# Performance work log

Hardware: AMD Instinct MI355X
Metric: run time of the kernel (lower is better)

## Reference

```python
import jax, jax.numpy as jnp
import numpy as np

NEG_SLOPE = 0.2


def gat_conv(h_in, src, dst, W, attn_l, attn_r, num_nodes):
    """DGL-style GATConv: fc -> per-head attention logits -> edge softmax over dst -> scatter-add."""
    H, D = attn_l.shape
    h = (h_in @ W).reshape(num_nodes, H, D)                      # [N,H,D]
    el = jnp.sum(h * attn_l, axis=-1)                            # [N,H]
    er = jnp.sum(h * attn_r, axis=-1)                            # [N,H]
    e = jax.nn.leaky_relu(el[src] + er[dst], NEG_SLOPE)          # [E,H]
    m = jax.ops.segment_max(e, dst, num_segments=num_nodes)      # [N,H]
    m = jnp.where(jnp.isfinite(m), m, 0.0)                       # guard empty segments
    ex = jnp.exp(e - m[dst])                                     # [E,H]
    denom = jax.ops.segment_sum(ex, dst, num_segments=num_nodes) # [N,H]
    a = ex / denom[dst]                                          # [E,H]
    msg = h[src] * a[:, :, None]                                 # [E,H,D]
    out = jax.ops.segment_sum(msg, dst, num_segments=num_nodes)  # [N,H,D]
    return out.reshape(num_nodes, H * D)                         # concat heads


def setup_inputs() -> dict:
    key = jax.random.key(0)
    ks = jax.random.split(key, 12)
    N, E, G = 65536, 1048576, 512
    F_in, H, D = 128, 8, 32
    F_mid = H * D  # 256, concat agg mode
    P = 512
    inp = {
        "node_feats": jax.random.normal(ks[0], (N, F_in), jnp.float32),
        "src": jax.random.randint(ks[1], (E,), 0, N, jnp.int32),
        "dst": jax.random.randint(ks[2], (E,), 0, N, jnp.int32),
        "graph_ids": jnp.sort(jax.random.randint(ks[3], (N,), 0, G, jnp.int32)),
        "num_graphs": G,
        "W0": jax.random.normal(ks[4], (F_in, H * D), jnp.float32) * (1.0 / np.sqrt(F_in)),
        "al0": jax.random.normal(ks[5], (H, D), jnp.float32) * 0.1,
        "ar0": jax.random.normal(ks[6], (H, D), jnp.float32) * 0.1,
        "W1": jax.random.normal(ks[7], (F_mid, H * D), jnp.float32) * (1.0 / np.sqrt(F_mid)),
        "al1": jax.random.normal(ks[8], (H, D), jnp.float32) * 0.1,
        "ar1": jax.random.normal(ks[9], (H, D), jnp.float32) * 0.1,
        "Wd1": jax.random.normal(ks[10], (F_mid, P), jnp.float32) * (1.0 / np.sqrt(F_mid)),
        "bd1": jnp.zeros((P,), jnp.float32),
        "Wd2": jax.random.normal(ks[11], (P, 1), jnp.float32) * (1.0 / np.sqrt(P)),
        "bd2": jnp.zeros((1,), jnp.float32),
    }
    return inp


def reference(node_feats, src, dst, graph_ids, num_graphs,
              W0, al0, ar0, W1, al1, ar1, Wd1, bd1, Wd2, bd2):
    N = node_feats.shape[0]
    # two GATConv message-passing steps with concat head aggregation
    h = gat_conv(node_feats, src, dst, W0, al0, ar0, N)   # [N, 256]
    h = gat_conv(h, src, dst, W1, al1, ar1, N)            # [N, 256]
    # mean readout per graph (AvgPooling)
    sums = jax.ops.segment_sum(h, graph_ids, num_segments=num_graphs)         # [G, 256]
    counts = jax.ops.segment_sum(jnp.ones((N,), h.dtype), graph_ids,
                                 num_segments=num_graphs)                     # [G]
    pooled = sums / jnp.maximum(counts, 1.0)[:, None]
    # predictor MLP: Dense(512, relu) -> Dense(1, linear)
    hidden = jax.nn.relu(pooled @ Wd1 + bd1)
    out = hidden @ Wd2 + bd2                               # [G, 1]
    return out
```

## Files before the change

### kernel.cpp

```cpp
#include <hip/hip_runtime.h>

#define LEAKY 0.2f

typedef unsigned short ushort_t;
typedef __attribute__((ext_vector_type(8))) short short8;
typedef __attribute__((ext_vector_type(4))) float f32x4;

__device__ __forceinline__ unsigned short f2bf(float f) {
  unsigned u = __float_as_uint(f);
  unsigned r = (u + 0x7fff + ((u >> 16) & 1)) >> 16;
  return (unsigned short)r;
}
__device__ __forceinline__ float bf2f(unsigned short u) {
  return __uint_as_float(((unsigned)u) << 16);
}

__global__ void count_k(const int* __restrict__ dst, int* __restrict__ cnt, int E) {
  int base = (blockIdx.x * blockDim.x + threadIdx.x) * 4;
  if (base + 3 < E) {
    int4 d = *(const int4*)(dst + base);
    atomicAdd(&cnt[d.x], 1);
    atomicAdd(&cnt[d.y], 1);
    atomicAdd(&cnt[d.z], 1);
    atomicAdd(&cnt[d.w], 1);
  } else {
    for (int i = base; i < E; ++i) atomicAdd(&cnt[dst[i]], 1);
  }
}

__global__ __launch_bounds__(1024) void scan1_k(int* __restrict__ cnt,
                                                int* __restrict__ ptr,
                                                int* __restrict__ bsum, int N) {
  int t = threadIdx.x;
  int i = blockIdx.x * 1024 + t;
  int v = (i < N) ? cnt[i] : 0;
  if (i < N) cnt[i] = 0;
  int lane = t & 63, w = t >> 6;
  int x = v;
  #pragma unroll
  for (int off = 1; off < 64; off <<= 1) {
    int y = __shfl_up(x, off, 64);
    if (lane >= off) x += y;
  }
  __shared__ int wsum[16];
  if (lane == 63) wsum[w] = x;
  __syncthreads();
  if (t < 16) {
    int s = wsum[t];
    #pragma unroll
    for (int off = 1; off < 16; off <<= 1) {
      int y = __shfl_up(s, off, 16);
      if (t >= off) s += y;
    }
    wsum[t] = s;
  }
  __syncthreads();
  int woff = (w > 0) ? wsum[w - 1] : 0;
  int incl = x + woff;
  if (i < N) ptr[i] = incl - v;
  if (t == 1023) bsum[blockIdx.x] = incl;
}

__global__ __launch_bounds__(1024) void scan23_k(int* __restrict__ ptr,
                                                 const int* __restrict__ bsum,
                                                 int nb, int N, int E) {
  __shared__ int sh[64];
  int t = threadIdx.x;
  if (t < 64) {
    int v = (t < nb) ? bsum[t] : 0;
    int x = v;
    #pragma unroll
    for (int off = 1; off < 64; off <<= 1) {
      int y = __shfl_up(x, off, 64);
      if (t >= off) x += y;
    }
    sh[t] = x - v;
  }
  __syncthreads();
  int i = blockIdx.x * 1024 + t;
  if (i < N) ptr[i] += sh[blockIdx.x];
  if (i == 0) ptr[N] = E;
}

__global__ void fill_k(const int* __restrict__ dst, const int* __restrict__ src,
                       const int* __restrict__ ptr, int* __restrict__ cur,
                       int* __restrict__ adj, int E) {
  int base = (blockIdx.x * blockDim.x + threadIdx.x) * 4;
  if (base + 3 < E) {
    int4 d = *(const int4*)(dst + base);
    int4 s = *(const int4*)(src + base);
    int p0 = atomicAdd(&cur[d.x], 1); adj[ptr[d.x] + p0] = s.x;
    int p1 = atomicAdd(&cur[d.y], 1); adj[ptr[d.y] + p1] = s.y;
    int p2 = atomicAdd(&cur[d.z], 1); adj[ptr[d.z] + p2] = s.z;
    int p3 = atomicAdd(&cur[d.w], 1); adj[ptr[d.w] + p3] = s.w;
  } else {
    for (int i = base; i < E; ++i) {
      int d = dst[i];
      int p = atomicAdd(&cur[d], 1);
      adj[ptr[d] + p] = src[i];
    }
  }
}

__global__ void wsplit2_k(const float* __restrict__ W0, const float* __restrict__ W1,
                          ushort_t* __restrict__ W0h, ushort_t* __restrict__ W1h) {
  int i = blockIdx.x * 256 + threadIdx.x;
  if (i < 256 * 128) {
    int k = i % 128, c = i / 128;
    W0h[i] = f2bf(W0[(long)k * 256 + c]);
  } else {
    int j = i - 256 * 128;
    if (j < 256 * 256) {
      int k = j % 256, c = j / 256;
      W1h[j] = f2bf(W1[(long)k * 256 + c]);
    }
  }
}

#define LDT 40
template <int AF32>
__global__ __launch_bounds__(256) void gemmT_k(const void* __restrict__ Ag_,
                                               const ushort_t* __restrict__ Bh,
                                               const float* __restrict__ alv,
                                               const float* __restrict__ arv,
                                               ushort_t* __restrict__ C,
                                               float* __restrict__ el,
                                               float* __restrict__ er,
                                               int N, int K) {
  __shared__ ushort_t smem[128 * LDT + 256 * LDT];
  ushort_t* As = smem;
  ushort_t* Bs = smem + 128 * LDT;
  int t = threadIdx.x;
  int w = t >> 6, l = t & 63;
  int wv_r = w >> 1, wv_c = w & 1;
  long row0 = (long)blockIdx.x * 128;
  int fr = l & 15;
  int ko = (l >> 4) * 8;
  int crow = (l >> 4) * 4;
  int ar = t >> 1;
  int ak = (t & 1) * 16;
  int bc = t;
  f32x4 acc[4][8] = {};

  for (int k0 = 0; k0 < K; k0 += 32) {
    ushort4 ha[4];
    uint4 a0, a1;
    if (AF32) {
      const float* ap = (const float*)Ag_ + (row0 + ar) * (long)K + k0 + ak;
      float4 v0 = *(const float4*)(ap + 0);
      float4 v1 = *(const float4*)(ap + 4);
      float4 v2 = *(const float4*)(ap + 8);
      float4 v3 = *(const float4*)(ap + 12);
      ha[0] = make_ushort4(f2bf(v0.x), f2bf(v0.y), f2bf(v0.z), f2bf(v0.w));
      ha[1] = make_ushort4(f2bf(v1.x), f2bf(v1.y), f2bf(v1.z), f2bf(v1.w));
      ha[2] = make_ushort4(f2bf(v2.x), f2bf(v2.y), f2bf(v2.z), f2bf(v2.w));
      ha[3] = make_ushort4(f2bf(v3.x), f2bf(v3.y), f2bf(v3.z), f2bf(v3.w));
    } else {
      const ushort_t* ap = (const ushort_t*)Ag_ + (row0 + ar) * (long)K + k0 + ak;
      a0 = *(const uint4*)ap;
      a1 = *(const uint4*)(ap + 8);
    }
    const ushort_t* bp = Bh + (long)bc * K + k0;
    uint4 b0 = *(const uint4*)bp;
    uint4 b1 = *(const uint4*)(bp + 8);
    uint4 b2 = *(const uint4*)(bp + 16);
    uint4 b3 = *(const uint4*)(bp + 24);
    __syncthreads();
    if (AF32) {
      *(ushort4*)&As[ar * LDT + ak + 0] = ha[0];
      *(ushort4*)&As[ar * LDT + ak + 4] = ha[1];
      *(ushort4*)&As[ar * LDT + ak + 8] = ha[2];
      *(ushort4*)&As[ar * LDT + ak + 12] = ha[3];
    } else {
      *(uint4*)&As[ar * LDT + ak] = a0;
      *(uint4*)&As[ar * LDT + ak + 8] = a1;
    }
    *(uint4*)&Bs[bc * LDT + 0] = b0;
    *(uint4*)&Bs[bc * LDT + 8] = b1;
    *(uint4*)&Bs[bc * LDT + 16] = b2;
    *(uint4*)&Bs[bc * LDT + 24] = b3;
    __syncthreads();
    short8 fah[4];
    #pragma unroll
    for (int m = 0; m < 4; ++m)
      fah[m] = *(const short8*)&As[(wv_r * 64 + m * 16 + fr) * LDT + ko];
    #pragma unroll
    for (int n = 0; n < 8; ++n) {
      short8 fb = *(const short8*)&Bs[(wv_c * 128 + n * 16 + fr) * LDT + ko];
      #pragma unroll
      for (int m = 0; m < 4; ++m)
        acc[m][n] = __builtin_amdgcn_mfma_f32_16x16x32_bf16(fah[m], fb, acc[m][n], 0, 0, 0);
    }
  }
  float ala[4], alb[4], ara[4], arb[4];
  #pragma unroll
  for (int hd = 0; hd < 4; ++hd) {
    int hbase = (wv_c * 4 + hd) * 32;
    ala[hd] = alv[hbase + fr];
    alb[hd] = alv[hbase + 16 + fr];
    ara[hd] = arv[hbase + fr];
    arb[hd] = arv[hbase + 16 + fr];
  }
  #pragma unroll
  for (int m = 0; m < 4; ++m) {
    #pragma unroll
    for (int r = 0; r < 4; ++r) {
      long row = row0 + wv_r * 64 + m * 16 + crow + r;
      #pragma unroll
      for (int n = 0; n < 8; ++n)
        C[row * 256 + wv_c * 128 + n * 16 + fr] = f2bf(acc[m][n][r]);
      #pragma unroll
      for (int hd = 0; hd < 4; ++hd) {
        float pel = acc[m][2 * hd][r] * ala[hd] + acc[m][2 * hd + 1][r] * alb[hd];
        float per = acc[m][2 * hd][r] * ara[hd] + acc[m][2 * hd + 1][r] * arb[hd];
        #pragma unroll
        for (int s = 1; s < 16; s <<= 1) {
          pel += __shfl_xor(pel, s);
          per += __shfl_xor(per, s);
        }
        if (fr == 0) {
          el[row * 8 + wv_c * 4 + hd] = pel;
          er[row * 8 + wv_c * 4 + hd] = per;
        }
      }
    }
  }
}

__global__ __launch_bounds__(256) void agg_k(const ushort_t* __restrict__ hb,
                                             const float* __restrict__ el,
                                             const float* __restrict__ er,
                                             const int* __restrict__ ptr,
                                             const int* __restrict__ adj,
                                             ushort_t* __restrict__ oh, int N) {
  int wid = threadIdx.x >> 6;
  int l = threadIdx.x & 63;
  int n = blockIdx.x * 4 + wid;
  if (n >= N) return;
  int beg = ptr[n];
  int deg = ptr[n + 1] - beg;
  long obase = (long)n * 256 + l * 4;
  float4 acc = make_float4(0.f, 0.f, 0.f, 0.f);
  if (deg > 0) {
    int hh = l & 7;
    int eo = l >> 3;
    int hg = l >> 3;
    float erv = er[(long)n * 8 + hh];
    if (deg <= 64) {
      int sid = (l < deg) ? adj[beg + l] : 0;
      int npass = (deg + 7) >> 3;
      float v[8];
      float m = -1e30f;
      #pragma unroll
      for (int p = 0; p < 8; ++p) {
        if (p < npass) {
          int e = p * 8 + eo;
          int s = __shfl(sid, e);
          float vv = -1e30f;
          if (e < deg) {
            vv = el[(long)s * 8 + hh] + erv;
            vv = vv > 0.f ? vv : LEAKY * vv;
          }
          v[p] = vv;
          m = fmaxf(m, vv);
        }
      }
      m = fmaxf(m, __shfl_xor(m, 8));
      m = fmaxf(m, __shfl_xor(m, 16));
      m = fmaxf(m, __shfl_xor(m, 32));
      float ssum = 0.f;
      #pragma unroll
      for (int p = 0; p < 8; ++p) {
        if (p < npass) {
          float ex = (p * 8 + eo < deg) ? __expf(v[p] - m) : 0.f;
          v[p] = ex;
          ssum += ex;
        }
      }
      ssum += __shfl_xor(ssum, 8);
      ssum += __shfl_xor(ssum, 16);
      ssum += __shfl_xor(ssum, 32);
      float inv = 1.0f / ssum;
      #pragma unroll
      for (int p = 0; p < 8; ++p) {
        if (p < npass) {
          v[p] *= inv;
          #pragma unroll
          for (int e2 = 0; e2 < 8; ++e2) {
            int e = p * 8 + e2;
            if (e < deg) {
              float a = __shfl(v[p], (e2 << 3) | hg);
              int s = __shfl(sid, e);
              const ushort4 hv = *(const ushort4*)(hb + (long)s * 256 + l * 4);
              acc.x += a * bf2f(hv.x);
              acc.y += a * bf2f(hv.y);
              acc.z += a * bf2f(hv.z);
              acc.w += a * bf2f(hv.w);
            }
          }
        }
      }
    } else {
      float m = -1e30f;
      for (int base = 0; base < deg; base += 8) {
        int e = base + eo;
        float vv = -1e30f;
        if (e < deg) {
          int s = adj[beg + e];
          vv = el[(long)s * 8 + hh] + erv;
          vv = vv > 0.f ? vv : LEAKY * vv;
        }
        m = fmaxf(m, vv);
      }
      m = fmaxf(m, __shfl_xor(m, 8));
      m = fmaxf(m, __shfl_xor(m, 16));
      m = fmaxf(m, __shfl_xor(m, 32));
      float ssum = 0.f;
      for (int base = 0; base < deg; base += 8) {
        int e = base + eo;
        if (e < deg) {
          int s = adj[beg + e];
          float vv = el[(long)s * 8 + hh] + erv;
          vv = vv > 0.f ? vv : LEAKY * vv;
          ssum += __expf(vv - m);
        }
      }
      ssum += __shfl_xor(ssum, 8);
      ssum += __shfl_xor(ssum, 16);
      ssum += __shfl_xor(ssum, 32);
      float inv = 1.0f / ssum;
      for (int base = 0; base < deg; base += 8) {
        int e = base + eo;
        float a_me = 0.f;
        int s_me = 0;
        if (e < deg) {
          s_me = adj[beg + e];
          float vv = el[(long)s_me * 8 + hh] + erv;
          vv = vv > 0.f ? vv : LEAKY * vv;
          a_me = __expf(vv - m) * inv;
        }
        #pragma unroll
        for (int e2 = 0; e2 < 8; ++e2) {
          int e3 = base + e2;
          if (e3 < deg) {
            int srcl = (e2 << 3) | hg;
            float a = __shfl(a_me, srcl);
            int s = __shfl(s_me, srcl);
            const ushort4 hv = *(const ushort4*)(hb + (long)s * 256 + l * 4);
            acc.x += a * bf2f(hv.x);
            acc.y += a * bf2f(hv.y);
            acc.z += a * bf2f(hv.z);
            acc.w += a * bf2f(hv.w);
          }
        }
      }
    }
  }
  *(ushort4*)(oh + obase) =
      make_ushort4(f2bf(acc.x), f2bf(acc.y), f2bf(acc.z), f2bf(acc.w));
}

__device__ __forceinline__ int lower_bound_i(const int* a, int n, int key) {
  int lo = 0, hi = n;
  while (lo < hi) {
    int mid = (lo + hi) >> 1;
    if (a[mid] < key) lo = mid + 1; else hi = mid;
  }
  return lo;
}

__global__ __launch_bounds__(256) void poolmlp_k(const ushort_t* __restrict__ h,
                                                 const int* __restrict__ gid,
                                                 const float* __restrict__ Wd1,
                                                 const float* __restrict__ bd1,
                                                 const float* __restrict__ Wd2,
                                                 const float* __restrict__ bd2,
                                                 float* __restrict__ outv, int N, int G) {
  int g = blockIdx.x;
  int t = threadIdx.x;
  __shared__ int s_lo, s_hi;
  if (t == 0) {
    s_lo = lower_bound_i(gid, N, g);
    s_hi = lower_bound_i(gid, N, g + 1);
  }
  __syncthreads();
  int lo = s_lo, hi = s_hi;
  float acc = 0.f;
  for (int n = lo; n < hi; ++n) acc += bf2f(h[(long)n * 256 + t]);
  float c = (float)(hi - lo);
  __shared__ float p_s[256];
  __shared__ float red[256];
  p_s[t] = acc / fmaxf(c, 1.f);
  __syncthreads();
  float acc0 = bd1[t], acc1 = bd1[t + 256];
  for (int k = 0; k < 256; ++k) {
    float pv = p_s[k];
    acc0 += pv * Wd1[k * 512 + t];
    acc1 += pv * Wd1[k * 512 + t + 256];
  }
  acc0 = fmaxf(acc0, 0.f);
  acc1 = fmaxf(acc1, 0.f);
  red[t] = acc0 * Wd2[t] + acc1 * Wd2[t + 256];
  __syncthreads();
  for (int off = 128; off > 0; off >>= 1) {
    if (t < off) red[t] += red[t + off];
    __syncthreads();
  }
  if (t == 0) outv[g] = red[0] + bd2[0];
}

extern "C" void kernel_launch(void* const* d_in, const int* in_sizes, int n_in,
                              void* d_out, int out_size, void* d_ws, size_t ws_size,
                              hipStream_t stream) {
  const float* X   = (const float*)d_in[0];
  const int*   src = (const int*)d_in[1];
  const int*   dst = (const int*)d_in[2];
  const int*   gid = (const int*)d_in[3];
  const float* W0  = (const float*)d_in[5];
  const float* al0 = (const float*)d_in[6];
  const float* ar0 = (const float*)d_in[7];
  const float* W1  = (const float*)d_in[8];
  const float* al1 = (const float*)d_in[9];
  const float* ar1 = (const float*)d_in[10];
  const float* Wd1 = (const float*)d_in[11];
  const float* bd1 = (const float*)d_in[12];
  const float* Wd2 = (const float*)d_in[13];
  const float* bd2 = (const float*)d_in[14];

  int E = in_sizes[1];
  int N = in_sizes[3];
  int G = out_size;

  char* p = (char*)d_ws;
  ushort_t* hb   = (ushort_t*)p; p += (size_t)N * 256 * 2;
  ushort_t* hagg = (ushort_t*)p; p += (size_t)N * 256 * 2;
  float*    el   = (float*)p;    p += (size_t)N * 8 * 4;
  float*    er   = (float*)p;    p += (size_t)N * 8 * 4;
  ushort_t* W0h  = (ushort_t*)p; p += (size_t)256 * 128 * 2;
  ushort_t* W1h  = (ushort_t*)p; p += (size_t)256 * 256 * 2;
  int*      ptr  = (int*)p;      p += (size_t)(N + 1) * 4;
  int*      cnt  = (int*)p;      p += (size_t)N * 4;
  int*      adj  = (int*)p;      p += (size_t)E * 4;
  int*      bsum = (int*)p;

  int nb = (N + 1023) / 1024;

  hipMemsetAsync(cnt, 0, (size_t)N * 4, stream);
  count_k<<<(E / 4 + 255) / 256, 256, 0, stream>>>(dst, cnt, E);
  scan1_k<<<nb, 1024, 0, stream>>>(cnt, ptr, bsum, N);
  scan23_k<<<nb, 1024, 0, stream>>>(ptr, bsum, nb, N, E);
  fill_k<<<(E / 4 + 255) / 256, 256, 0, stream>>>(dst, src, ptr, cnt, adj, E);

  wsplit2_k<<<(256 * 128 + 256 * 256 + 255) / 256, 256, 0, stream>>>(W0, W1, W0h, W1h);

  gemmT_k<1><<<N / 128, 256, 0, stream>>>((const void*)X, W0h, al0, ar0, hb, el, er, N, 128);
  agg_k<<<(N + 3) / 4, 256, 0, stream>>>(hb, el, er, ptr, adj, hagg, N);
  gemmT_k<0><<<N / 128, 256, 0, stream>>>((const void*)hagg, W1h, al1, ar1, hb, el, er, N, 256);
  agg_k<<<(N + 3) / 4, 256, 0, stream>>>(hb, el, er, ptr, adj, hagg, N);
  poolmlp_k<<<G, 256, 0, stream>>>(hagg, gid, Wd1, bd1, Wd2, bd2, (float*)d_out, N, G);
}
```

Baseline: 451.5 us.

## Record edge slots in count pass, fuse prep kernels, stage attention in LDS

The count kernel now saves each edge's atomic return value as its slot, so the fill kernel scatters without a second round of atomics. The memset and weight-conversion kernel are merged into a single prep kernel, which removes launches. In the aggregation kernel, normalised attention weights and source ids go to shared memory and are read back per edge, replacing the cross-lane shuffles. Leaky ReLU becomes an fmax. The cost is an extra E-sized slot buffer that is written and then read again. The prep grid is sized by N, which covers the weight sizes only when N is at least 65536.

```diff
diff --git a/kernel.cpp b/kernel.cpp
--- a/kernel.cpp
+++ b/kernel.cpp
@@ -15,26 +15,45 @@
   return __uint_as_float(((unsigned)u) << 16);
 }
 
-__global__ void count_k(const int* __restrict__ dst, int* __restrict__ cnt, int E) {
+__global__ __launch_bounds__(256) void prep_k(int* __restrict__ cnt,
+                                              const float* __restrict__ W0,
+                                              const float* __restrict__ W1,
+                                              ushort_t* __restrict__ W0h,
+                                              ushort_t* __restrict__ W1h, int N) {
+  int i = blockIdx.x * 256 + threadIdx.x;
+  if (i < N) cnt[i] = 0;
+  if (i < 256 * 128) {
+    int k = i % 128, c = i / 128;
+    W0h[i] = f2bf(W0[(long)k * 256 + c]);
+  }
+  if (i < 256 * 256) {
+    int k = i % 256, c = i / 256;
+    W1h[i] = f2bf(W1[(long)k * 256 + c]);
+  }
+}
+
+__global__ void count_k(const int* __restrict__ dst, int* __restrict__ cnt,
+                        int* __restrict__ slot, int E) {
   int base = (blockIdx.x * blockDim.x + threadIdx.x) * 4;
   if (base + 3 < E) {
     int4 d = *(const int4*)(dst + base);
-    atomicAdd(&cnt[d.x], 1);
-    atomicAdd(&cnt[d.y], 1);
-    atomicAdd(&cnt[d.z], 1);
-    atomicAdd(&cnt[d.w], 1);
+    int4 s;
+    s.x = atomicAdd(&cnt[d.x], 1);
+    s.y = atomicAdd(&cnt[d.y], 1);
+    s.z = atomicAdd(&cnt[d.z], 1);
+    s.w = atomicAdd(&cnt[d.w], 1);
+    *(int4*)(slot + base) = s;
   } else {
-    for (int i = base; i < E; ++i) atomicAdd(&cnt[dst[i]], 1);
-  }
-}
-
-__global__ __launch_bounds__(1024) void scan1_k(int* __restrict__ cnt,
+    for (int i = base; i < E; ++i) slot[i] = atomicAdd(&cnt[dst[i]], 1);
+  }
+}
+
+__global__ __launch_bounds__(1024) void scan1_k(const int* __restrict__ cnt,
                                                 int* __restrict__ ptr,
                                                 int* __restrict__ bsum, int N) {
   int t = threadIdx.x;
   int i = blockIdx.x * 1024 + t;
   int v = (i < N) ? cnt[i] : 0;
-  if (i < N) cnt[i] = 0;
   int lane = t & 63, w = t >> 6;
   int x = v;
   #pragma unroll
@@ -83,37 +102,19 @@
 }
 
 __global__ void fill_k(const int* __restrict__ dst, const int* __restrict__ src,
-                       const int* __restrict__ ptr, int* __restrict__ cur,
+                       const int* __restrict__ slot, const int* __restrict__ ptr,
                        int* __restrict__ adj, int E) {
   int base = (blockIdx.x * blockDim.x + threadIdx.x) * 4;
   if (base + 3 < E) {
     int4 d = *(const int4*)(dst + base);
     int4 s = *(const int4*)(src + base);
-    int p0 = atomicAdd(&cur[d.x], 1); adj[ptr[d.x] + p0] = s.x;
-    int p1 = atomicAdd(&cur[d.y], 1); adj[ptr[d.y] + p1] = s.y;
-    int p2 = atomicAdd(&cur[d.z], 1); adj[ptr[d.z] + p2] = s.z;
-    int p3 = atomicAdd(&cur[d.w], 1); adj[ptr[d.w] + p3] = s.w;
+    int4 q = *(const int4*)(slot + base);
+    adj[ptr[d.x] + q.x] = s.x;
+    adj[ptr[d.y] + q.y] = s.y;
+    adj[ptr[d.z] + q.z] = s.z;
+    adj[ptr[d.w] + q.w] = s.w;
   } else {
-    for (int i = base; i < E; ++i) {
-      int d = dst[i];
-      int p = atomicAdd(&cur[d], 1);
-      adj[ptr[d] + p] = src[i];
-    }
-  }
-}
-
-__global__ void wsplit2_k(const float* __restrict__ W0, const float* __restrict__ W1,
-                          ushort_t* __restrict__ W0h, ushort_t* __restrict__ W1h) {
-  int i = blockIdx.x * 256 + threadIdx.x;
-  if (i < 256 * 128) {
-    int k = i % 128, c = i / 128;
-    W0h[i] = f2bf(W0[(long)k * 256 + c]);
-  } else {
-    int j = i - 256 * 128;
-    if (j < 256 * 256) {
-      int k = j % 256, c = j / 256;
-      W1h[j] = f2bf(W1[(long)k * 256 + c]);
-    }
+    for (int i = base; i < E; ++i) adj[ptr[dst[i]] + slot[i]] = src[i];
   }
 }
 
@@ -233,6 +234,7 @@
                                              const int* __restrict__ ptr,
                                              const int* __restrict__ adj,
                                              ushort_t* __restrict__ oh, int N) {
+  __shared__ float2 att[4][64][8];
   int wid = threadIdx.x >> 6;
   int l = threadIdx.x & 63;
   int n = blockIdx.x * 4 + wid;
@@ -250,16 +252,18 @@
       int sid = (l < deg) ? adj[beg + l] : 0;
       int npass = (deg + 7) >> 3;
       float v[8];
+      int sv[8];
       float m = -1e30f;
       #pragma unroll
       for (int p = 0; p < 8; ++p) {
         if (p < npass) {
           int e = p * 8 + eo;
           int s = __shfl(sid, e);
+          sv[p] = s;
           float vv = -1e30f;
           if (e < deg) {
             vv = el[(long)s * 8 + hh] + erv;
-            vv = vv > 0.f ? vv : LEAKY * vv;
+            vv = fmaxf(vv, LEAKY * vv);
           }
           v[p] = vv;
           m = fmaxf(m, vv);
@@ -284,19 +288,24 @@
       #pragma unroll
       for (int p = 0; p < 8; ++p) {
         if (p < npass) {
-          v[p] *= inv;
-          #pragma unroll
-          for (int e2 = 0; e2 < 8; ++e2) {
-            int e = p * 8 + e2;
-            if (e < deg) {
-              float a = __shfl(v[p], (e2 << 3) | hg);
-              int s = __shfl(sid, e);
-              const ushort4 hv = *(const ushort4*)(hb + (long)s * 256 + l * 4);
-              acc.x += a * bf2f(hv.x);
-              acc.y += a * bf2f(hv.y);
-              acc.z += a * bf2f(hv.z);
-              acc.w += a * bf2f(hv.w);
-            }
+          int e = p * 8 + eo;
+          if (e < deg)
+            att[wid][e][hh] = make_float2(v[p] * inv, __int_as_float(sv[p]));
+        }
+      }
+      for (int p = 0; p < npass; ++p) {
+        #pragma unroll
+        for (int e2 = 0; e2 < 8; ++e2) {
+          int e = p * 8 + e2;
+          if (e < deg) {
+            float2 as_ = att[wid][e][hg];
+            float a = as_.x;
+            int s = __float_as_int(as_.y);
+            const ushort4 hv = *(const ushort4*)(hb + (long)s * 256 + l * 4);
+            acc.x += a * bf2f(hv.x);
+            acc.y += a * bf2f(hv.y);
+            acc.z += a * bf2f(hv.z);
+            acc.w += a * bf2f(hv.w);
           }
         }
       }
@@ -308,7 +317,7 @@
         if (e < deg) {
           int s = adj[beg + e];
           vv = el[(long)s * 8 + hh] + erv;
-          vv = vv > 0.f ? vv : LEAKY * vv;
+          vv = fmaxf(vv, LEAKY * vv);
         }
         m = fmaxf(m, vv);
       }
@@ -321,7 +330,7 @@
         if (e < deg) {
           int s = adj[beg + e];
           float vv = el[(long)s * 8 + hh] + erv;
-          vv = vv > 0.f ? vv : LEAKY * vv;
+          vv = fmaxf(vv, LEAKY * vv);
           ssum += __expf(vv - m);
         }
       }
@@ -336,7 +345,7 @@
         if (e < deg) {
           s_me = adj[beg + e];
           float vv = el[(long)s_me * 8 + hh] + erv;
-          vv = vv > 0.f ? vv : LEAKY * vv;
+          vv = fmaxf(vv, LEAKY * vv);
           a_me = __expf(vv - m) * inv;
         }
         #pragma unroll
@@ -441,17 +450,16 @@
   int*      ptr  = (int*)p;      p += (size_t)(N + 1) * 4;
   int*      cnt  = (int*)p;      p += (size_t)N * 4;
   int*      adj  = (int*)p;      p += (size_t)E * 4;
+  int*      slot = (int*)p;      p += (size_t)E * 4;
   int*      bsum = (int*)p;
 
   int nb = (N + 1023) / 1024;
 
-  hipMemsetAsync(cnt, 0, (size_t)N * 4, stream);
-  count_k<<<(E / 4 + 255) / 256, 256, 0, stream>>>(dst, cnt, E);
+  prep_k<<<(N + 255) / 256, 256, 0, stream>>>(cnt, W0, W1, W0h, W1h, N);
+  count_k<<<(E / 4 + 255) / 256, 256, 0, stream>>>(dst, cnt, slot, E);
   scan1_k<<<nb, 1024, 0, stream>>>(cnt, ptr, bsum, N);
   scan23_k<<<nb, 1024, 0, stream>>>(ptr, bsum, nb, N, E);
-  fill_k<<<(E / 4 + 255) / 256, 256, 0, stream>>>(dst, src, ptr, cnt, adj, E);
-
-  wsplit2_k<<<(256 * 128 + 256 * 256 + 255) / 256, 256, 0, stream>>>(W0, W1, W0h, W1h);
+  fill_k<<<(E / 4 + 255) / 256, 256, 0, stream>>>(dst, src, slot, ptr, adj, E);
 
   gemmT_k<1><<<N / 128, 256, 0, stream>>>((const void*)X, W0h, al0, ar0, hb, el, er, N, 128);
   agg_k<<<(N + 3) / 4, 256, 0, stream>>>(hb, el, er, ptr, adj, hagg, N);
```

New measurement: 415.5 us. 1.09x faster.
